# Kernel tuning notes

Measured on AMD Instinct MI355X. Metric: run time of the kernel, lower is better.

## Reference

```python
import jax, jax.numpy as jnp
import numpy as np

EMB = 256
HEADS = 2
IMG = 224
P1, P2 = 16, 8
LN_EPS = 1e-5


def _layer_norm(t, g, b):
    m = jnp.mean(t, axis=-1, keepdims=True)
    v = jnp.mean((t - m) ** 2, axis=-1, keepdims=True)
    return (t - m) * jax.lax.rsqrt(v + LN_EPS) * g + b


def _patch_embed(x, W, b, cls_tok, p):
    B, C, H, Wd = x.shape
    h, w = H // p, Wd // p
    # b c (h p1)(w p2) -> b (h w) (p1 p2 c)
    t = x.reshape(B, C, h, p, w, p).transpose(0, 2, 4, 3, 5, 1).reshape(B, h * w, p * p * C)
    t = t @ W + b
    cls = jnp.broadcast_to(cls_tok, (B, 1, cls_tok.shape[-1]))
    return jnp.concatenate([cls, t], axis=1)


def setup_inputs() -> dict:
    key = jax.random.key(0)
    ks = jax.random.split(key, 16)
    s = 0.02
    d = {
        "x": jax.random.normal(ks[0], (128, 3, IMG, IMG), dtype=jnp.float32),
        "W1": jax.random.normal(ks[1], (P1 * P1 * 3, EMB), dtype=jnp.float32) * s,
        "b1": jnp.zeros((EMB,), jnp.float32),
        "cls1": jax.random.normal(ks[2], (1, 1, EMB), dtype=jnp.float32),
        "W2": jax.random.normal(ks[3], (P2 * P2 * 3, EMB), dtype=jnp.float32) * s,
        "b2": jnp.zeros((EMB,), jnp.float32),
        "cls2": jax.random.normal(ks[4], (1, 1, EMB), dtype=jnp.float32),
        "ln1_g": jnp.ones((EMB,), jnp.float32),
        "ln1_b": jnp.zeros((EMB,), jnp.float32),
        "Wq": jax.random.normal(ks[5], (EMB, EMB), dtype=jnp.float32) * s,
        "bq": jnp.zeros((EMB,), jnp.float32),
        "Wk": jax.random.normal(ks[6], (EMB, EMB), dtype=jnp.float32) * s,
        "bk": jnp.zeros((EMB,), jnp.float32),
        "Wv": jax.random.normal(ks[7], (EMB, EMB), dtype=jnp.float32) * s,
        "bv": jnp.zeros((EMB,), jnp.float32),
        "Wp": jax.random.normal(ks[8], (EMB, EMB), dtype=jnp.float32) * s,
        "bp": jnp.zeros((EMB,), jnp.float32),
        "ln2_g": jnp.ones((EMB,), jnp.float32),
        "ln2_b": jnp.zeros((EMB,), jnp.float32),
        "lnc_g": jnp.ones((EMB,), jnp.float32),
        "lnc_b": jnp.zeros((EMB,), jnp.float32),
        "Wc": jax.random.normal(ks[9], (EMB, 2), dtype=jnp.float32) * s,
        "bc": jnp.zeros((2,), jnp.float32),
    }
    return d


def reference(x, W1, b1, cls1, W2, b2, cls2, ln1_g, ln1_b, Wq, bq, Wk, bk, Wv, bv,
              Wp, bp, ln2_g, ln2_b, lnc_g, lnc_b, Wc, bc):
    B = x.shape[0]
    p1 = _patch_embed(x, W1, b1, cls1, P1)   # [B, 197, 256]
    p2 = _patch_embed(x, W2, b2, cls2, P2)   # [B, 785, 256]
    n = p1.shape[1]
    idx = jnp.linspace(0.0, p2.shape[1] - 1, n).astype(jnp.int32)  # truncation like .long()
    p2r = p2[:, idx, :]
    z = jnp.concatenate([p2r, p1], axis=1)   # [B, 394, 256]
    N = z.shape[1]

    h = _layer_norm(z, ln1_g, ln1_b)
    dh = EMB // HEADS
    q = (h @ Wq + bq).reshape(B, N, HEADS, dh).transpose(0, 2, 1, 3)
    k = (h @ Wk + bk).reshape(B, N, HEADS, dh).transpose(0, 2, 1, 3)
    v = (h @ Wv + bv).reshape(B, N, HEADS, dh).transpose(0, 2, 1, 3)
    attn = jnp.einsum('bhqd,bhkd->bhqk', q, k)
    # NOTE: faithful to source — softmax of UNscaled logits, then divide by sqrt(emb)
    attn = jax.nn.softmax(attn, axis=-1) / (EMB ** 0.5)
    o = jnp.einsum('bhqk,bhkd->bhqd', attn, v).transpose(0, 2, 1, 3).reshape(B, N, EMB)
    o = o @ Wp + bp
    o = _layer_norm(o, ln2_g, ln2_b)
    z = z + o

    pooled = jnp.mean(z, axis=1)
    logits = _layer_norm(pooled, lnc_g, lnc_b) @ Wc + bc
    return jax.nn.log_softmax(logits, axis=1)
```

## Files before the change

kernel.cpp:

```cpp
#include <hip/hip_runtime.h>

typedef short short8 __attribute__((ext_vector_type(8)));
typedef float f32x4 __attribute__((ext_vector_type(4)));
typedef unsigned short us4 __attribute__((ext_vector_type(4)));
typedef unsigned short u16;

#define MFMA(a,b,c) __builtin_amdgcn_mfma_f32_16x16x32_bf16((a),(b),(c),0,0,0)

__device__ __forceinline__ u16 f2b(float f) {
    union { float f; unsigned int i; } v; v.f = f;
    unsigned int x = v.i;
    return (u16)((x + 0x7fffu + ((x >> 16) & 1u)) >> 16);
}

__device__ __forceinline__ unsigned int pk2(float lo, float hi) {
    return (unsigned int)f2b(lo) | ((unsigned int)f2b(hi) << 16);
}

__global__ __launch_bounds__(256) void k_wtrans(const float* __restrict__ W1,
        const float* __restrict__ W2, const float* __restrict__ Wq, const float* __restrict__ Wk,
        const float* __restrict__ Wv, const float* __restrict__ Wp,
        u16* __restrict__ w1t, u16* __restrict__ w2t, u16* __restrict__ wqt,
        u16* __restrict__ wkt, u16* __restrict__ wvt, u16* __restrict__ wpt) {
    int bx = blockIdx.x, n = threadIdx.x;
    if (bx < 768) {
        int k = bx, c = k % 3, t = k / 3, pj = t & 15, pi = t >> 4;
        int kp2 = c*256 + pi*16 + pj;
        w1t[(size_t)(kp2 >> 5)*8192 + n*32 + (kp2 & 31)] = f2b(W1[(size_t)k*256 + n]);
    } else if (bx < 960) {
        int k = bx - 768, c = k % 3, t = k / 3, pj = t & 7, pi = t >> 3;
        int kp2 = c*64 + pi*8 + pj;
        w2t[(size_t)(kp2 >> 5)*8192 + n*32 + (kp2 & 31)] = f2b(W2[(size_t)k*256 + n]);
    } else if (bx < 1216) { int k = bx - 960;  wqt[(size_t)(k>>5)*8192 + n*32 + (k&31)] = f2b(Wq[(size_t)k*256 + n]); }
    else if (bx < 1472)   { int k = bx - 1216; wkt[(size_t)(k>>5)*8192 + n*32 + (k&31)] = f2b(Wk[(size_t)k*256 + n]); }
    else if (bx < 1728)   { int k = bx - 1472; wvt[(size_t)(k>>5)*8192 + n*32 + (k&31)] = f2b(Wv[(size_t)k*256 + n]); }
    else                  { int k = bx - 1728; wpt[(size_t)(k>>5)*8192 + n*32 + (k&31)] = f2b(Wp[(size_t)k*256 + n]); }
}

__global__ __launch_bounds__(256) void k_cls(const float* __restrict__ cls1,
        const float* __restrict__ cls2, const float* __restrict__ g1, const float* __restrict__ be1,
        float* __restrict__ z, u16* __restrict__ h) {
    __shared__ float red[16];
    int b = blockIdx.x, e = threadIdx.x, lane = e & 63, w = e >> 6;
    float v0 = cls2[e], v1 = cls1[e];
    z[((size_t)b*394 + 0)*256 + e]   = v0;
    z[((size_t)b*394 + 197)*256 + e] = v1;
    float s0 = v0, q0 = v0*v0, s1 = v1, q1 = v1*v1;
    #pragma unroll
    for (int m = 1; m < 64; m <<= 1) {
        s0 += __shfl_xor(s0, m); q0 += __shfl_xor(q0, m);
        s1 += __shfl_xor(s1, m); q1 += __shfl_xor(q1, m);
    }
    if (lane == 0) { red[w] = s0; red[4+w] = q0; red[8+w] = s1; red[12+w] = q1; }
    __syncthreads();
    float S0 = red[0]+red[1]+red[2]+red[3],   Q0 = red[4]+red[5]+red[6]+red[7];
    float S1 = red[8]+red[9]+red[10]+red[11], Q1 = red[12]+red[13]+red[14]+red[15];
    float m0 = S0*(1.f/256.f), r0 = rsqrtf(Q0*(1.f/256.f) - m0*m0 + 1e-5f);
    float m1 = S1*(1.f/256.f), r1 = rsqrtf(Q1*(1.f/256.f) - m1*m1 + 1e-5f);
    h[((size_t)b*394 + 0)*256 + e]   = f2b((v0-m0)*r0*g1[e] + be1[e]);
    h[((size_t)b*394 + 197)*256 + e] = f2b((v1-m1)*r1*g1[e] + be1[e]);
}

__global__ __launch_bounds__(256) void k_im2col1(const float* __restrict__ x,
        u16* __restrict__ A1) {
    int b = blockIdx.y, g = blockIdx.x, tid = threadIdx.x;
    int p = tid >> 4, pi = tid & 15;
    int j = g*16 + p;
    u16* dst = A1 + ((size_t)b*208 + j)*768;
    if (j < 196) {
        int hi = j / 14, wi = j - hi*14;
        #pragma unroll
        for (int c = 0; c < 3; ++c) {
            const float* src = x + (((size_t)b*3 + c)*224 + hi*16 + pi)*224 + wi*16;
            f32x4 r0 = *(const f32x4*)(src);
            f32x4 r1 = *(const f32x4*)(src + 4);
            f32x4 r2 = *(const f32x4*)(src + 8);
            f32x4 r3 = *(const f32x4*)(src + 12);
            union { u16 u[16]; uint4 q[2]; } t;
            #pragma unroll
            for (int s = 0; s < 4; ++s) {
                t.u[s] = f2b(r0[s]); t.u[4+s] = f2b(r1[s]);
                t.u[8+s] = f2b(r2[s]); t.u[12+s] = f2b(r3[s]);
            }
            *(uint4*)&dst[c*256 + pi*16] = t.q[0];
            *(uint4*)&dst[c*256 + pi*16 + 8] = t.q[1];
        }
    } else {
        uint4 zer = {0,0,0,0};
        #pragma unroll
        for (int c = 0; c < 3; ++c) {
            *(uint4*)&dst[c*256 + pi*16] = zer;
            *(uint4*)&dst[c*256 + pi*16 + 8] = zer;
        }
    }
}

__global__ __launch_bounds__(256) void k_embed1(const u16* __restrict__ A1,
        const u16* __restrict__ w1t, const float* __restrict__ b1,
        const float* __restrict__ g1, const float* __restrict__ be1,
        float* __restrict__ z, u16* __restrict__ h, int nrows) {
    __shared__ __align__(16) u16 Ab[2][64*40];
    __shared__ __align__(16) u16 Bb[2][256*40];
    __shared__ float red[64][8];
    int tid = threadIdx.x;
    int r0 = blockIdx.x * 64;
    int w = tid >> 6, lane = tid & 63, quad = lane >> 4, tf = lane & 15;
    int arow = tid >> 2, aoff = (tid & 3) * 8;
    const u16* ap = A1 + (size_t)(r0 + arow)*768 + aoff;
    uint4 ra  = *(const uint4*)(ap);
    uint4 rb0 = *(const uint4*)&w1t[tid*8];
    uint4 rb1 = *(const uint4*)&w1t[2048 + tid*8];
    uint4 rb2 = *(const uint4*)&w1t[4096 + tid*8];
    uint4 rb3 = *(const uint4*)&w1t[6144 + tid*8];
    f32x4 zero = {0.f,0.f,0.f,0.f};
    f32x4 acc[4][4];
    #pragma unroll
    for (int m = 0; m < 4; ++m)
        #pragma unroll
        for (int nf = 0; nf < 4; ++nf) acc[m][nf] = zero;
    #pragma unroll
    for (int kc = 0; kc < 24; ++kc) {
        int buf = kc & 1;
        *(uint4*)&Ab[buf][arow*40 + aoff] = ra;
        *(uint4*)&Bb[buf][(arow      )*40 + aoff] = rb0;
        *(uint4*)&Bb[buf][(arow +  64)*40 + aoff] = rb1;
        *(uint4*)&Bb[buf][(arow + 128)*40 + aoff] = rb2;
        *(uint4*)&Bb[buf][(arow + 192)*40 + aoff] = rb3;
        int nc = kc < 23 ? kc + 1 : 23;
        ra = *(const uint4*)(ap + nc*32);
        const u16* src = w1t + (size_t)nc*8192;
        rb0 = *(const uint4*)&src[tid*8];
        rb1 = *(const uint4*)&src[2048 + tid*8];
        rb2 = *(const uint4*)&src[4096 + tid*8];
        rb3 = *(const uint4*)&src[6144 + tid*8];
        __syncthreads();
        short8 a0 = *(const short8*)&Ab[buf][(     tf)*40 + quad*8];
        short8 a1 = *(const short8*)&Ab[buf][(16 + tf)*40 + quad*8];
        short8 a2 = *(const short8*)&Ab[buf][(32 + tf)*40 + quad*8];
        short8 a3 = *(const short8*)&Ab[buf][(48 + tf)*40 + quad*8];
        #pragma unroll
        for (int nf = 0; nf < 4; ++nf) {
            short8 bb = *(const short8*)&Bb[buf][(w*64 + nf*16 + tf)*40 + quad*8];
            acc[0][nf] = MFMA(a0, bb, acc[0][nf]);
            acc[1][nf] = MFMA(a1, bb, acc[1][nf]);
            acc[2][nf] = MFMA(a2, bb, acc[2][nf]);
            acc[3][nf] = MFMA(a3, bb, acc[3][nf]);
        }
    }
    float bias[4], gv[4], bev[4];
    #pragma unroll
    for (int nf = 0; nf < 4; ++nf) {
        int n = w*64 + nf*16 + tf;
        bias[nf] = b1[n]; gv[nf] = g1[n]; bev[nf] = be1[n];
    }
    #pragma unroll
    for (int m = 0; m < 4; ++m)
        #pragma unroll
        for (int nf = 0; nf < 4; ++nf)
            #pragma unroll
            for (int i = 0; i < 4; ++i) acc[m][nf][i] += bias[nf];
    #pragma unroll
    for (int m = 0; m < 4; ++m)
        #pragma unroll
        for (int i = 0; i < 4; ++i) {
            float s = acc[m][0][i] + acc[m][1][i] + acc[m][2][i] + acc[m][3][i];
            float qv = acc[m][0][i]*acc[m][0][i] + acc[m][1][i]*acc[m][1][i]
                     + acc[m][2][i]*acc[m][2][i] + acc[m][3][i]*acc[m][3][i];
            #pragma unroll
            for (int d = 1; d < 16; d <<= 1) { s += __shfl_xor(s, d); qv += __shfl_xor(qv, d); }
            if (tf == 0) {
                red[m*16 + quad*4 + i][w] = s;
                red[m*16 + quad*4 + i][4 + w] = qv;
            }
        }
    __syncthreads();
    #pragma unroll
    for (int m = 0; m < 4; ++m)
        #pragma unroll
        for (int i = 0; i < 4; ++i) {
            int rl = m*16 + quad*4 + i;
            float S = red[rl][0]+red[rl][1]+red[rl][2]+red[rl][3];
            float Q = red[rl][4]+red[rl][5]+red[rl][6]+red[rl][7];
            float mean = S*(1.f/256.f);
            float rs = rsqrtf(Q*(1.f/256.f) - mean*mean + 1e-5f);
            int row = r0 + rl;
            if (row < nrows) {
                int img = row / 208;
                int j = row - img*208;
                if (j < 196) {
                    size_t base = ((size_t)img*394 + 198 + j)*256;
                    #pragma unroll
                    for (int nf = 0; nf < 4; ++nf) {
                        int n = w*64 + nf*16 + tf;
                        float v = acc[m][nf][i];
                        z[base + n] = v;
                        h[base + n] = f2b((v - mean)*rs*gv[nf] + bev[nf]);
                    }
                }
            }
        }
}

__global__ __launch_bounds__(256) void k_embed2(const float* __restrict__ x,
        const u16* __restrict__ w2t, const float* __restrict__ b2,
        const float* __restrict__ g1, const float* __restrict__ be1,
        float* __restrict__ z, u16* __restrict__ h) {
    __shared__ __align__(16) u16 A[16*200];
    __shared__ __align__(16) u16 Wst[8192];
    __shared__ __align__(16) float S[16*260];
    int b = blockIdx.y, g = blockIdx.x, tid = threadIdx.x;
    int p = tid >> 4, s16 = tid & 15;
    int pi = s16 >> 1, ph = s16 & 1;
    int it = g*16 + p + 1;
    uint4 wr0 = *(const uint4*)&w2t[tid*8];
    uint4 wr1 = *(const uint4*)&w2t[2048 + tid*8];
    uint4 wr2 = *(const uint4*)&w2t[4096 + tid*8];
    uint4 wr3 = *(const uint4*)&w2t[6144 + tid*8];
    auto stage = [&](const u16* base, int chunk) {
        __syncthreads();
        *(uint4*)&Wst[tid*8] = wr0;
        *(uint4*)&Wst[2048 + tid*8] = wr1;
        *(uint4*)&Wst[4096 + tid*8] = wr2;
        *(uint4*)&Wst[6144 + tid*8] = wr3;
        __syncthreads();
        if (base) {
            const u16* src = base + (size_t)chunk*8192;
            wr0 = *(const uint4*)&src[tid*8];
            wr1 = *(const uint4*)&src[2048 + tid*8];
            wr2 = *(const uint4*)&src[4096 + tid*8];
            wr3 = *(const uint4*)&src[6144 + tid*8];
        }
    };
    if (it <= 196) {
        int patch = 4*it - 1;
        int hi = patch / 28, wi = patch - hi*28;
        #pragma unroll
        for (int c = 0; c < 3; ++c) {
            const float* src = x + (((size_t)b*3 + c)*224 + hi*8 + pi)*224 + wi*8 + ph*4;
            f32x4 r = *(const f32x4*)src;
            us4 o; o[0] = f2b(r[0]); o[1] = f2b(r[1]); o[2] = f2b(r[2]); o[3] = f2b(r[3]);
            *(us4*)&A[p*200 + c*64 + pi*8 + ph*4] = o;
        }
    } else {
        us4 zer = {0,0,0,0};
        #pragma unroll
        for (int c = 0; c < 3; ++c)
            *(us4*)&A[p*200 + c*64 + pi*8 + ph*4] = zer;
    }
    int w = tid >> 6, lane = tid & 63, quad = lane >> 4, tf = lane & 15;
    f32x4 zero = {0.f,0.f,0.f,0.f};
    f32x4 acc[4] = {zero,zero,zero,zero};
    #pragma unroll
    for (int ks = 0; ks < 6; ++ks) {
        stage(ks < 5 ? w2t : nullptr, ks + 1);
        short8 a = *(const short8*)&A[tf*200 + ks*32 + quad*8];
        #pragma unroll
        for (int nf = 0; nf < 4; ++nf) {
            short8 bb = *(const short8*)&Wst[(w*64 + nf*16 + tf)*32 + quad*8];
            acc[nf] = MFMA(a, bb, acc[nf]);
        }
    }
    #pragma unroll
    for (int nf = 0; nf < 4; ++nf) {
        int n = w*64 + nf*16 + tf;
        float bias = b2[n];
        #pragma unroll
        for (int i = 0; i < 4; ++i)
            S[(quad*4 + i)*260 + n] = acc[nf][i] + bias;
    }
    __syncthreads();
    #pragma unroll
    for (int rr = 0; rr < 4; ++rr) {
        int row = w*4 + rr;
        int it2 = g*16 + row + 1;
        f32x4 v = *(const f32x4*)&S[row*260 + lane*4];
        float s = v[0]+v[1]+v[2]+v[3];
        float sq = v[0]*v[0]+v[1]*v[1]+v[2]*v[2]+v[3]*v[3];
        #pragma unroll
        for (int m = 1; m < 64; m <<= 1) { s += __shfl_xor(s, m); sq += __shfl_xor(sq, m); }
        float mean = s*(1.f/256.f);
        float rs = rsqrtf(sq*(1.f/256.f) - mean*mean + 1e-5f);
        if (it2 <= 196) {
            size_t base = ((size_t)b*394 + it2)*256 + lane*4;
            *(f32x4*)&z[base] = v;
            us4 ho;
            #pragma unroll
            for (int c = 0; c < 4; ++c) {
                int e = lane*4 + c;
                ho[c] = f2b((v[c]-mean)*rs*g1[e] + be1[e]);
            }
            *(us4*)&h[base] = ho;
        }
    }
}

__device__ __forceinline__ void store_qk(f32x4 acc[4][4], const float* __restrict__ bs,
        u16* __restrict__ dst, u16* Sst, int b, int mt, int w, int quad, int tf, int tid) {
    #pragma unroll
    for (int m = 0; m < 4; ++m) {
        __syncthreads();
        #pragma unroll
        for (int nf = 0; nf < 4; ++nf) {
            int e = w*64 + nf*16 + tf;
            float bias = bs[e];
            #pragma unroll
            for (int i = 0; i < 4; ++i) {
                int n = mt*64 + m*16 + quad*4 + i;
                Sst[(quad*4 + i)*264 + e] = (n < 394) ? f2b(acc[m][nf][i] + bias) : (u16)0;
            }
        }
        __syncthreads();
        int row = tid >> 4, c16 = tid & 15;
        int n = mt*64 + m*16 + row;
        if (n < 416) {
            int e0 = c16*16, hh = e0 >> 7, d0 = e0 & 127;
            uint4 v0 = *(const uint4*)&Sst[row*264 + e0];
            uint4 v1 = *(const uint4*)&Sst[row*264 + e0 + 8];
            u16* p = dst + ((size_t)(b*2 + hh)*416 + n)*128 + d0;
            *(uint4*)p = v0;
            *(uint4*)(p + 8) = v1;
        }
    }
}

__device__ __forceinline__ void store_v(f32x4 acc[4][4], const float* __restrict__ bs,
        u16* __restrict__ vt, u16* Sst, int b, int mt, int w, int quad, int tf, int tid) {
    #pragma unroll
    for (int nf = 0; nf < 4; ++nf) {
        __syncthreads();
        #pragma unroll
        for (int i = 0; i < 4; ++i) {
            int e = w*64 + nf*16 + quad*4 + i;
            float bias = bs[e];
            #pragma unroll
            for (int m = 0; m < 4; ++m) {
                int n = mt*64 + m*16 + tf;
                Sst[(w*16 + quad*4 + i)*72 + m*16 + tf] = (n < 394) ? f2b(acc[m][nf][i] + bias) : (u16)0;
            }
        }
        __syncthreads();
        #pragma unroll
        for (int k = 0; k < 2; ++k) {
            int ch = tid + k*256;
            int row = ch >> 3, c8 = ch & 7;
            int n0 = mt*64 + c8*8;
            if (n0 < 416) {
                int e = (row >> 4)*64 + nf*16 + (row & 15);
                int d = e & 127, hh = e >> 7;
                uint4 v = *(const uint4*)&Sst[row*72 + c8*8];
                *(uint4*)&vt[((size_t)(b*2 + hh)*128 + d)*416 + n0] = v;
            }
        }
    }
}

__global__ __launch_bounds__(256) void k_qkv(const u16* __restrict__ h,
        const u16* __restrict__ wqt, const u16* __restrict__ wkt, const u16* __restrict__ wvt,
        const float* __restrict__ bq, const float* __restrict__ bk, const float* __restrict__ bv,
        u16* __restrict__ q, u16* __restrict__ kb, u16* __restrict__ vt) {
    __shared__ __align__(16) u16 A[64*264];
    __shared__ __align__(16) u16 Wst[2][8192];
    __shared__ __align__(16) u16 Sst[4608];
    int mt = blockIdx.x, b = blockIdx.y, tid = threadIdx.x;
    auto cptr = [&](int i) -> const u16* {
        return i < 8 ? wqt + (size_t)i*8192
             : i < 16 ? wkt + (size_t)(i-8)*8192
                      : wvt + (size_t)(i-16)*8192;
    };
    uint4 wa0, wa1, wa2, wa3;
    uint4 wb0, wb1, wb2, wb3;
    auto loadA = [&](const u16* src) {
        wa0 = *(const uint4*)&src[tid*8];
        wa1 = *(const uint4*)&src[2048 + tid*8];
        wa2 = *(const uint4*)&src[4096 + tid*8];
        wa3 = *(const uint4*)&src[6144 + tid*8];
    };
    auto loadB = [&](const u16* src) {
        wb0 = *(const uint4*)&src[tid*8];
        wb1 = *(const uint4*)&src[2048 + tid*8];
        wb2 = *(const uint4*)&src[4096 + tid*8];
        wb3 = *(const uint4*)&src[6144 + tid*8];
    };
    auto writeA = [&]() {
        *(uint4*)&Wst[0][tid*8] = wa0;
        *(uint4*)&Wst[0][2048 + tid*8] = wa1;
        *(uint4*)&Wst[0][4096 + tid*8] = wa2;
        *(uint4*)&Wst[0][6144 + tid*8] = wa3;
    };
    auto writeB = [&]() {
        *(uint4*)&Wst[1][tid*8] = wb0;
        *(uint4*)&Wst[1][2048 + tid*8] = wb1;
        *(uint4*)&Wst[1][4096 + tid*8] = wb2;
        *(uint4*)&Wst[1][6144 + tid*8] = wb3;
    };
    loadA(cptr(0));
    loadB(cptr(1));
    #pragma unroll
    for (int it = 0; it < 8; ++it) {
        int idx = tid + it*256;
        int row = idx >> 5, seg = idx & 31;
        int n = mt*64 + row;
        uint4 val = {0,0,0,0};
        if (n < 394) val = *(const uint4*)&h[((size_t)b*394 + n)*256 + seg*8];
        *(uint4*)&A[row*264 + seg*8] = val;
    }
    int w = tid >> 6, lane = tid & 63, quad = lane >> 4, tf = lane & 15;
    f32x4 zero = {0.f,0.f,0.f,0.f};

    {
        f32x4 acc[4][4];
        #pragma unroll
        for (int m = 0; m < 4; ++m)
            #pragma unroll
            for (int nf = 0; nf < 4; ++nf) acc[m][nf] = zero;
        #pragma unroll
        for (int ks = 0; ks < 8; ++ks) {
            int i = ks, buf = ks & 1;
            if (buf == 0) writeA(); else writeB();
            if (i + 2 < 24) { if (buf == 0) loadA(cptr(i + 2)); else loadB(cptr(i + 2)); }
            __syncthreads();
            short8 a0 = *(const short8*)&A[tf*264 + ks*32 + quad*8];
            short8 a1 = *(const short8*)&A[(16+tf)*264 + ks*32 + quad*8];
            short8 a2 = *(const short8*)&A[(32+tf)*264 + ks*32 + quad*8];
            short8 a3 = *(const short8*)&A[(48+tf)*264 + ks*32 + quad*8];
            #pragma unroll
            for (int nf = 0; nf < 4; ++nf) {
                short8 bb = *(const short8*)&Wst[buf][(w*64 + nf*16 + tf)*32 + quad*8];
                acc[0][nf] = MFMA(a0, bb, acc[0][nf]);
                acc[1][nf] = MFMA(a1, bb, acc[1][nf]);
                acc[2][nf] = MFMA(a2, bb, acc[2][nf]);
                acc[3][nf] = MFMA(a3, bb, acc[3][nf]);
            }
        }
        store_qk(acc, bq, q, Sst, b, mt, w, quad, tf, tid);
    }
    {
        f32x4 acc[4][4];
        #pragma unroll
        for (int m = 0; m < 4; ++m)
            #pragma unroll
            for (int nf = 0; nf < 4; ++nf) acc[m][nf] = zero;
        #pragma unroll
        for (int ks = 0; ks < 8; ++ks) {
            int i = 8 + ks, buf = ks & 1;
            if (buf == 0) writeA(); else writeB();
            if (i + 2 < 24) { if (buf == 0) loadA(cptr(i + 2)); else loadB(cptr(i + 2)); }
            __syncthreads();
            short8 a0 = *(const short8*)&A[tf*264 + ks*32 + quad*8];
            short8 a1 = *(const short8*)&A[(16+tf)*264 + ks*32 + quad*8];
            short8 a2 = *(const short8*)&A[(32+tf)*264 + ks*32 + quad*8];
            short8 a3 = *(const short8*)&A[(48+tf)*264 + ks*32 + quad*8];
            #pragma unroll
            for (int nf = 0; nf < 4; ++nf) {
                short8 bb = *(const short8*)&Wst[buf][(w*64 + nf*16 + tf)*32 + quad*8];
                acc[0][nf] = MFMA(a0, bb, acc[0][nf]);
                acc[1][nf] = MFMA(a1, bb, acc[1][nf]);
                acc[2][nf] = MFMA(a2, bb, acc[2][nf]);
                acc[3][nf] = MFMA(a3, bb, acc[3][nf]);
            }
        }
        store_qk(acc, bk, kb, Sst, b, mt, w, quad, tf, tid);
    }
    {
        f32x4 acc[4][4];
        #pragma unroll
        for (int m = 0; m < 4; ++m)
            #pragma unroll
            for (int nf = 0; nf < 4; ++nf) acc[m][nf] = zero;
        #pragma unroll
        for (int ks = 0; ks < 8; ++ks) {
            int i = 16 + ks, buf = ks & 1;
            if (buf == 0) writeA(); else writeB();
            if (i + 2 < 24) { if (buf == 0) loadA(cptr(i + 2)); else loadB(cptr(i + 2)); }
            __syncthreads();
            short8 a0 = *(const short8*)&A[tf*264 + ks*32 + quad*8];
            short8 a1 = *(const short8*)&A[(16+tf)*264 + ks*32 + quad*8];
            short8 a2 = *(const short8*)&A[(32+tf)*264 + ks*32 + quad*8];
            short8 a3 = *(const short8*)&A[(48+tf)*264 + ks*32 + quad*8];
            #pragma unroll
            for (int nf = 0; nf < 4; ++nf) {
                short8 bb = *(const short8*)&Wst[buf][(w*64 + nf*16 + tf)*32 + quad*8];
                acc[0][nf] = MFMA(bb, a0, acc[0][nf]);
                acc[1][nf] = MFMA(bb, a1, acc[1][nf]);
                acc[2][nf] = MFMA(bb, a2, acc[2][nf]);
                acc[3][nf] = MFMA(bb, a3, acc[3][nf]);
            }
        }
        store_v(acc, bv, vt, Sst, b, mt, w, quad, tf, tid);
    }
}

__global__ __launch_bounds__(256) void k_att(const u16* __restrict__ q,
        const u16* __restrict__ kbuf, const u16* __restrict__ vt, u16* __restrict__ o) {
    __shared__ __align__(16) u16 pool[18944];
    int nwg = gridDim.x * gridDim.y;
    int orig = blockIdx.y * gridDim.x + blockIdx.x;
    int q8 = nwg >> 3, r8 = nwg & 7;
    int xcd = orig & 7, idx = orig >> 3;
    int nid = (xcd < r8 ? xcd*(q8+1) : r8*(q8+1) + (xcd-r8)*q8) + idx;
    int bx = nid % 7, bh = nid / 7;
    int tid = threadIdx.x;
    int w = tid >> 6, lane = tid & 63, quad = lane >> 4, tf = lane & 15;
    int mt_raw = bx*4 + w;
    int mt = mt_raw < 26 ? mt_raw : 25;
    const u16* qp = q    + (size_t)bh*53248;
    const u16* kp = kbuf + (size_t)bh*53248;
    const u16* vp = vt   + (size_t)bh*53248;
    short8 afr[4];
    #pragma unroll
    for (int ks = 0; ks < 4; ++ks)
        afr[ks] = *(const short8*)&qp[(size_t)(mt*16 + tf)*128 + ks*32 + quad*8];
    f32x4 zero = {0.f,0.f,0.f,0.f};
    f32x4 acc[25];
    #pragma unroll
    for (int nt = 0; nt < 25; ++nt) acc[nt] = zero;
    int sr0 = tid >> 4, sseg = tid & 15;
    uint4 kreg0 = *(const uint4*)&kp[(size_t)sr0*128 + sseg*8];
    uint4 kreg1 = *(const uint4*)&kp[(size_t)(sr0+16)*128 + sseg*8];
    for (int kc = 0; kc < 13; ++kc) {
        u16* K = pool + (kc & 1)*4352;
        *(uint4*)&K[sr0*136 + sseg*8] = kreg0;
        *(uint4*)&K[(sr0+16)*136 + sseg*8] = kreg1;
        if (kc < 12) {
            kreg0 = *(const uint4*)&kp[(size_t)((kc+1)*32 + sr0)*128 + sseg*8];
            kreg1 = *(const uint4*)&kp[(size_t)((kc+1)*32 + sr0 + 16)*128 + sseg*8];
        }
        __syncthreads();
        #pragma unroll
        for (int ncl = 0; ncl < 2; ++ncl) {
            int nt = kc*2 + ncl;
            if (nt < 25) {
                #pragma unroll
                for (int ks = 0; ks < 4; ++ks) {
                    short8 kk = *(const short8*)&K[(ncl*16 + tf)*136 + ks*32 + quad*8];
                    acc[nt] = MFMA(kk, afr[ks], acc[nt]);
                }
            }
        }
    }
    int vd0 = tid >> 2, vseg = tid & 3;
    uint4 vreg0 = *(const uint4*)&vp[(size_t)vd0*416 + vseg*8];
    uint4 vreg1 = *(const uint4*)&vp[(size_t)(vd0+64)*416 + vseg*8];
    float mx = -3e38f;
    #pragma unroll
    for (int nt = 0; nt < 24; ++nt)
        #pragma unroll
        for (int i = 0; i < 4; ++i) mx = fmaxf(mx, acc[nt][i]);
    #pragma unroll
    for (int i = 0; i < 4; ++i)
        if (quad*4 + i < 10) mx = fmaxf(mx, acc[24][i]);
    mx = fmaxf(mx, __shfl_xor(mx, 16));
    mx = fmaxf(mx, __shfl_xor(mx, 32));
    float s = 0.f;
    #pragma unroll
    for (int nt = 0; nt < 24; ++nt)
        #pragma unroll
        for (int i = 0; i < 4; ++i) {
            float e = __expf(acc[nt][i] - mx);
            acc[nt][i] = e; s += e;
        }
    #pragma unroll
    for (int i = 0; i < 4; ++i) {
        if (quad*4 + i < 10) { float e = __expf(acc[24][i] - mx); acc[24][i] = e; s += e; }
        else acc[24][i] = 0.f;
    }
    s += __shfl_xor(s, 16);
    s += __shfl_xor(s, 32);
    float inv = 1.f / (16.f * s);
    #pragma unroll
    for (int nt = 0; nt < 25; ++nt)
        #pragma unroll
        for (int i = 0; i < 4; ++i) acc[nt][i] *= inv;
    f32x4 acc2[8];
    #pragma unroll
    for (int nf = 0; nf < 8; ++nf) acc2[nf] = zero;
    int qb0 = quad & 1;
    int g = (qb0 << 1) | (quad >> 1);
    for (int kc = 0; kc < 13; ++kc) {
        u16* V = pool + 8704 + (kc & 1)*5120;
        *(uint4*)&V[vd0*40 + vseg*8] = vreg0;
        *(uint4*)&V[(vd0+64)*40 + vseg*8] = vreg1;
        if (kc < 12) {
            vreg0 = *(const uint4*)&vp[(size_t)vd0*416 + (kc+1)*32 + vseg*8];
            vreg1 = *(const uint4*)&vp[(size_t)(vd0+64)*416 + (kc+1)*32 + vseg*8];
        }
        __syncthreads();
        f32x4 v0 = acc[2*kc];
        f32x4 v1 = (kc < 12) ? acc[2*kc + 1] : zero;
        unsigned int r0 = pk2(v0[0], v0[1]);
        unsigned int r1 = pk2(v0[2], v0[3]);
        unsigned int r2 = pk2(v1[0], v1[1]);
        unsigned int r3 = pk2(v1[2], v1[3]);
        unsigned int sa = qb0 ? r0 : r2, sb = qb0 ? r1 : r3;
        unsigned int ra = (unsigned int)__shfl_xor((int)sa, 16);
        unsigned int rb = (unsigned int)__shfl_xor((int)sb, 16);
        unsigned int ka = qb0 ? r2 : r0, kb2 = qb0 ? r3 : r1;
        union { unsigned int u[4]; short8 s8; } au;
        au.u[0] = qb0 ? ra : ka;
        au.u[1] = qb0 ? rb : kb2;
        au.u[2] = qb0 ? ka : ra;
        au.u[3] = qb0 ? kb2 : rb;
        short8 a = au.s8;
        #pragma unroll
        for (int nf = 0; nf < 8; ++nf) {
            short8 bb = *(const short8*)&V[(nf*16 + tf)*40 + g*8];
            acc2[nf] = MFMA(a, bb, acc2[nf]);
        }
    }
    int b = bh >> 1, hh = bh & 1;
    __syncthreads();
    #pragma unroll
    for (int nf = 0; nf < 8; ++nf)
        #pragma unroll
        for (int i = 0; i < 4; ++i)
            pool[w*2176 + (quad*4 + i)*136 + nf*16 + tf] = f2b(acc2[nf][i]);
    __syncthreads();
    if (mt_raw < 26) {
        #pragma unroll
        for (int r4 = 0; r4 < 4; ++r4) {
            int rr = r4*4 + (lane >> 4);
            int n = mt_raw*16 + rr;
            if (n < 394) {
                int c16 = lane & 15;
                uint4 v = *(const uint4*)&pool[w*2176 + rr*136 + c16*8];
                *(uint4*)&o[((size_t)b*394 + n)*256 + hh*128 + c16*8] = v;
            }
        }
    }
}

__global__ __launch_bounds__(256) void k_proj(const u16* __restrict__ o,
        const u16* __restrict__ wpt, const float* __restrict__ bp,
        const float* __restrict__ g2, const float* __restrict__ bb2,
        float* __restrict__ z) {
    __shared__ __align__(16) u16 A[32*264];
    __shared__ __align__(16) u16 Wst[8192];
    __shared__ __align__(16) float S[32*260];
    int mt = blockIdx.x, b = blockIdx.y, tid = threadIdx.x;
    int w = tid >> 6, lane = tid & 63, quad = lane >> 4, tf = lane & 15;
    uint4 wr0 = *(const uint4*)&wpt[tid*8];
    uint4 wr1 = *(const uint4*)&wpt[2048 + tid*8];
    uint4 wr2 = *(const uint4*)&wpt[4096 + tid*8];
    uint4 wr3 = *(const uint4*)&wpt[6144 + tid*8];
    auto stage = [&](const u16* base, int chunk) {
        __syncthreads();
        *(uint4*)&Wst[tid*8] = wr0;
        *(uint4*)&Wst[2048 + tid*8] = wr1;
        *(uint4*)&Wst[4096 + tid*8] = wr2;
        *(uint4*)&Wst[6144 + tid*8] = wr3;
        __syncthreads();
        if (base) {
            const u16* src = base + (size_t)chunk*8192;
            wr0 = *(const uint4*)&src[tid*8];
            wr1 = *(const uint4*)&src[2048 + tid*8];
            wr2 = *(const uint4*)&src[4096 + tid*8];
            wr3 = *(const uint4*)&src[6144 + tid*8];
        }
    };
    for (int idx = tid; idx < 2048; idx += 256) {
        int row = idx >> 6, col4 = (idx & 63) * 4;
        int n = mt*32 + row;
        us4 val = {0,0,0,0};
        if (n < 394) val = *(const us4*)&o[((size_t)b*394 + n)*256 + col4];
        *(us4*)&A[row*264 + col4] = val;
    }
    f32x4 zero = {0.f,0.f,0.f,0.f};
    f32x4 acc[2][4];
    #pragma unroll
    for (int m = 0; m < 2; ++m)
        #pragma unroll
        for (int nf = 0; nf < 4; ++nf) acc[m][nf] = zero;
    #pragma unroll
    for (int ks = 0; ks < 8; ++ks) {
        stage(ks < 7 ? wpt : nullptr, ks + 1);
        short8 a0 = *(const short8*)&A[tf*264 + ks*32 + quad*8];
        short8 a1 = *(const short8*)&A[(16+tf)*264 + ks*32 + quad*8];
        #pragma unroll
        for (int nf = 0; nf < 4; ++nf) {
            short8 bb = *(const short8*)&Wst[(w*64 + nf*16 + tf)*32 + quad*8];
            acc[0][nf] = MFMA(a0, bb, acc[0][nf]);
            acc[1][nf] = MFMA(a1, bb, acc[1][nf]);
        }
    }
    #pragma unroll
    for (int nf = 0; nf < 4; ++nf) {
        int e = w*64 + nf*16 + tf;
        float bsv = bp[e];
        #pragma unroll
        for (int m = 0; m < 2; ++m)
            #pragma unroll
            for (int i = 0; i < 4; ++i)
                S[(m*16 + quad*4 + i)*260 + e] = acc[m][nf][i] + bsv;
    }
    __syncthreads();
    #pragma unroll
    for (int rr = 0; rr < 8; ++rr) {
        int row = w*8 + rr;
        f32x4 v = *(const f32x4*)&S[row*260 + lane*4];
        float s = v[0]+v[1]+v[2]+v[3];
        float sq = v[0]*v[0]+v[1]*v[1]+v[2]*v[2]+v[3]*v[3];
        #pragma unroll
        for (int m = 1; m < 64; m <<= 1) { s += __shfl_xor(s, m); sq += __shfl_xor(sq, m); }
        float mean = s*(1.f/256.f);
        float rs = rsqrtf(sq*(1.f/256.f) - mean*mean + 1e-5f);
        int n = mt*32 + row;
        if (n < 394) {
            float* zr = z + ((size_t)b*394 + n)*256 + lane*4;
            f32x4 zv = *(f32x4*)zr;
            #pragma unroll
            for (int c = 0; c < 4; ++c) {
                int e = lane*4 + c;
                zv[c] += (v[c]-mean)*rs*g2[e] + bb2[e];
            }
            *(f32x4*)zr = zv;
        }
    }
}

__global__ __launch_bounds__(256) void k_poolsum(const float* __restrict__ z,
        float* __restrict__ partial) {
    int g = blockIdx.x, b = blockIdx.y, e = threadIdx.x;
    int nb = gridDim.y;
    int n0 = g*99, n1 = 394 < n0+99 ? 394 : n0+99;
    const float* zp = z + (size_t)b*394*256 + e;
    float p0 = 0.f, p1 = 0.f, p2 = 0.f, p3 = 0.f;
    int n = n0;
    for (; n + 3 < n1; n += 4) {
        p0 += zp[(size_t)n*256];       p1 += zp[(size_t)(n+1)*256];
        p2 += zp[(size_t)(n+2)*256];   p3 += zp[(size_t)(n+3)*256];
    }
    for (; n < n1; ++n) p0 += zp[(size_t)n*256];
    partial[((size_t)g*nb + b)*256 + e] = (p0+p1)+(p2+p3);
}

__global__ __launch_bounds__(256) void k_pool2(const float* __restrict__ partial,
        const float* __restrict__ lg, const float* __restrict__ lb,
        const float* __restrict__ wc, const float* __restrict__ bc,
        float* __restrict__ out, int nb) {
    __shared__ float red[8];
    int b = blockIdx.x, e = threadIdx.x;
    int wave = e >> 6, lane = e & 63;
    float pooled = (partial[((size_t)0*nb + b)*256 + e] + partial[((size_t)1*nb + b)*256 + e]
                  + partial[((size_t)2*nb + b)*256 + e] + partial[((size_t)3*nb + b)*256 + e])
                 * (1.f/394.f);
    float a = pooled, sq = pooled*pooled;
    #pragma unroll
    for (int m = 1; m < 64; m <<= 1) { a += __shfl_xor(a, m); sq += __shfl_xor(sq, m); }
    if (lane == 0) { red[wave] = a; red[4+wave] = sq; }
    __syncthreads();
    float tot = red[0]+red[1]+red[2]+red[3];
    float totq = red[4]+red[5]+red[6]+red[7];
    float mean = tot*(1.f/256.f);
    float rs = rsqrtf(totq*(1.f/256.f) - mean*mean + 1e-5f);
    float ln = (pooled-mean)*rs*lg[e] + lb[e];
    float t0 = ln * wc[e*2], t1 = ln * wc[e*2+1];
    #pragma unroll
    for (int m = 1; m < 64; m <<= 1) { t0 += __shfl_xor(t0, m); t1 += __shfl_xor(t1, m); }
    __syncthreads();
    if (lane == 0) { red[wave] = t0; red[4+wave] = t1; }
    __syncthreads();
    if (e < 2) {
        float l0 = red[0]+red[1]+red[2]+red[3] + bc[0];
        float l1 = red[4]+red[5]+red[6]+red[7] + bc[1];
        float mx = fmaxf(l0, l1);
        float lse = mx + logf(__expf(l0-mx) + __expf(l1-mx));
        out[b*2 + e] = (e == 0 ? l0 : l1) - lse;
    }
}

extern "C" void kernel_launch(void* const* d_in, const int* in_sizes, int n_in,
                              void* d_out, int out_size, void* d_ws, size_t ws_size,
                              hipStream_t stream) {
    const float* x    = (const float*)d_in[0];
    const float* W1   = (const float*)d_in[1];
    const float* b1   = (const float*)d_in[2];
    const float* cls1 = (const float*)d_in[3];
    const float* W2   = (const float*)d_in[4];
    const float* b2   = (const float*)d_in[5];
    const float* cls2 = (const float*)d_in[6];
    const float* ln1g = (const float*)d_in[7];
    const float* ln1b = (const float*)d_in[8];
    const float* Wq   = (const float*)d_in[9];
    const float* bq   = (const float*)d_in[10];
    const float* Wk   = (const float*)d_in[11];
    const float* bk   = (const float*)d_in[12];
    const float* Wv   = (const float*)d_in[13];
    const float* bv   = (const float*)d_in[14];
    const float* Wp   = (const float*)d_in[15];
    const float* bp   = (const float*)d_in[16];
    const float* ln2g = (const float*)d_in[17];
    const float* ln2b = (const float*)d_in[18];
    const float* lncg = (const float*)d_in[19];
    const float* lncb = (const float*)d_in[20];
    const float* Wc   = (const float*)d_in[21];
    const float* bcp  = (const float*)d_in[22];

    int Bn = in_sizes[0] / (3*224*224);

    const size_t WBYTES = 1015808;
    const size_t PER_IMG = 403456 + 201728 + 212992*3 + 4096;
    size_t avail = (ws_size > WBYTES) ? ws_size - WBYTES : 0;
    int Bc = (int)(avail / PER_IMG);
    if (Bc < 1) Bc = 1;
    if (Bc > Bn) Bc = Bn;

    u16* w1t = (u16*)d_ws;
    u16* w2t = w1t + 196608;
    u16* wqt = w2t + 49152;
    u16* wkt = wqt + 65536;
    u16* wvt = wkt + 65536;
    u16* wpt = wvt + 65536;
    float* z = (float*)(wpt + 65536);
    u16* h   = (u16*)(z + (size_t)Bc*100864);
    u16* o   = h;
    u16* q   = h + (size_t)Bc*100864;
    u16* kb  = q + (size_t)Bc*106496;
    u16* vt  = kb + (size_t)Bc*106496;
    float* partial = (float*)(vt + (size_t)Bc*106496);

    k_wtrans<<<1984, 256, 0, stream>>>(W1, W2, Wq, Wk, Wv, Wp, w1t, w2t, wqt, wkt, wvt, wpt);

    for (int b0 = 0; b0 < Bn; b0 += Bc) {
        int bc = (Bn - b0 < Bc) ? (Bn - b0) : Bc;
        const float* xb = x + (size_t)b0 * 3*224*224;
        float* outb = (float*)d_out + (size_t)b0 * 2;
        int nrows = bc * 208;
        int gm = (nrows + 63) / 64;

        k_cls<<<bc, 256, 0, stream>>>(cls1, cls2, ln1g, ln1b, z, h);
        k_im2col1<<<dim3(13, bc), 256, 0, stream>>>(xb, q );
        k_embed1<<<gm, 256, 0, stream>>>(q , w1t, b1, ln1g, ln1b, z, h, nrows);
        k_embed2<<<dim3(13, bc), 256, 0, stream>>>(xb, w2t, b2, ln1g, ln1b, z, h);
        k_qkv<<<dim3(7, bc), 256, 0, stream>>>(h, wqt, wkt, wvt, bq, bk, bv, q, kb, vt);
        k_att<<<dim3(7, bc*2), 256, 0, stream>>>(q, kb, vt, o);
        k_proj<<<dim3(13, bc), 256, 0, stream>>>(o, wpt, bp, ln2g, ln2b, z);
        k_poolsum<<<dim3(4, bc), 256, 0, stream>>>(z, partial);
        k_pool2<<<bc, 256, 0, stream>>>(partial, lncg, lncb, Wc, bcp, outb, bc);
    }
}
```

Baseline: 376.5 us.

## Fuse both im2col gathers and run embed2 as row-tiled GEMM like embed1

The im2col kernel now also gathers the 8x8 patches needed for the second embedding into a separate bf16 buffer, reusing the vt scratch. k_embed2 becomes a double-buffered 32-row-tile GEMM mirroring k_embed1 with an in-register LayerNorm reduction, replacing the per-image 16-row tile that staged the full weights with two syncs per k-step. k_embed1's row tile is halved from 64 to 32 rows to launch more blocks. This trades an extra global write and read of the A2 buffer, and more weight reloads per row, for better occupancy and fewer barriers.

```diff
diff --git a/kernel.cpp b/kernel.cpp
--- a/kernel.cpp
+++ b/kernel.cpp
@@ -61,14 +61,16 @@
     h[((size_t)b*394 + 197)*256 + e] = f2b((v1-m1)*r1*g1[e] + be1[e]);
 }
 
-__global__ __launch_bounds__(256) void k_im2col1(const float* __restrict__ x,
-        u16* __restrict__ A1) {
+__global__ __launch_bounds__(256) void k_im2col(const float* __restrict__ x,
+        u16* __restrict__ A1, u16* __restrict__ A2) {
     int b = blockIdx.y, g = blockIdx.x, tid = threadIdx.x;
-    int p = tid >> 4, pi = tid & 15;
+    int p = tid >> 4, s16 = tid & 15;
     int j = g*16 + p;
-    u16* dst = A1 + ((size_t)b*208 + j)*768;
+    u16* dst  = A1 + ((size_t)b*208 + j)*768;
+    u16* dst2 = A2 + ((size_t)b*208 + j)*192;
     if (j < 196) {
         int hi = j / 14, wi = j - hi*14;
+        int pi = s16;
         #pragma unroll
         for (int c = 0; c < 3; ++c) {
             const float* src = x + (((size_t)b*3 + c)*224 + hi*16 + pi)*224 + wi*16;
@@ -85,12 +87,25 @@
             *(uint4*)&dst[c*256 + pi*16] = t.q[0];
             *(uint4*)&dst[c*256 + pi*16 + 8] = t.q[1];
         }
+        int patch = 4*j + 3;
+        int hi2 = patch / 28, wi2 = patch - hi2*28;
+        int pi2 = s16 >> 1, ph = s16 & 1;
+        #pragma unroll
+        for (int c = 0; c < 3; ++c) {
+            const float* src = x + (((size_t)b*3 + c)*224 + hi2*8 + pi2)*224 + wi2*8 + ph*4;
+            f32x4 r = *(const f32x4*)src;
+            us4 o; o[0] = f2b(r[0]); o[1] = f2b(r[1]); o[2] = f2b(r[2]); o[3] = f2b(r[3]);
+            *(us4*)&dst2[c*64 + pi2*8 + ph*4] = o;
+        }
     } else {
-        uint4 zer = {0,0,0,0};
+        uint4 zer4 = {0,0,0,0};
+        us4 zer = {0,0,0,0};
+        int pi = s16, pi2 = s16 >> 1, ph = s16 & 1;
         #pragma unroll
         for (int c = 0; c < 3; ++c) {
-            *(uint4*)&dst[c*256 + pi*16] = zer;
-            *(uint4*)&dst[c*256 + pi*16 + 8] = zer;
+            *(uint4*)&dst[c*256 + pi*16] = zer4;
+            *(uint4*)&dst[c*256 + pi*16 + 8] = zer4;
+            *(us4*)&dst2[c*64 + pi2*8 + ph*4] = zer;
         }
     }
 }
@@ -99,35 +114,36 @@
         const u16* __restrict__ w1t, const float* __restrict__ b1,
         const float* __restrict__ g1, const float* __restrict__ be1,
         float* __restrict__ z, u16* __restrict__ h, int nrows) {
-    __shared__ __align__(16) u16 Ab[2][64*40];
+    __shared__ __align__(16) u16 Ab[2][32*40];
     __shared__ __align__(16) u16 Bb[2][256*40];
-    __shared__ float red[64][8];
+    __shared__ float red[32][8];
     int tid = threadIdx.x;
-    int r0 = blockIdx.x * 64;
+    int r0 = blockIdx.x * 32;
     int w = tid >> 6, lane = tid & 63, quad = lane >> 4, tf = lane & 15;
-    int arow = tid >> 2, aoff = (tid & 3) * 8;
-    const u16* ap = A1 + (size_t)(r0 + arow)*768 + aoff;
-    uint4 ra  = *(const uint4*)(ap);
+    int arow = tid >> 3, aseg = (tid & 7) * 4;
+    int brow = tid >> 2, boff = (tid & 3) * 8;
+    const u16* ap = A1 + (size_t)(r0 + arow)*768 + aseg;
+    uint2 ra  = *(const uint2*)(ap);
     uint4 rb0 = *(const uint4*)&w1t[tid*8];
     uint4 rb1 = *(const uint4*)&w1t[2048 + tid*8];
     uint4 rb2 = *(const uint4*)&w1t[4096 + tid*8];
     uint4 rb3 = *(const uint4*)&w1t[6144 + tid*8];
     f32x4 zero = {0.f,0.f,0.f,0.f};
-    f32x4 acc[4][4];
-    #pragma unroll
-    for (int m = 0; m < 4; ++m)
+    f32x4 acc[2][4];
+    #pragma unroll
+    for (int m = 0; m < 2; ++m)
         #pragma unroll
         for (int nf = 0; nf < 4; ++nf) acc[m][nf] = zero;
     #pragma unroll
     for (int kc = 0; kc < 24; ++kc) {
         int buf = kc & 1;
-        *(uint4*)&Ab[buf][arow*40 + aoff] = ra;
-        *(uint4*)&Bb[buf][(arow      )*40 + aoff] = rb0;
-        *(uint4*)&Bb[buf][(arow +  64)*40 + aoff] = rb1;
-        *(uint4*)&Bb[buf][(arow + 128)*40 + aoff] = rb2;
-        *(uint4*)&Bb[buf][(arow + 192)*40 + aoff] = rb3;
+        *(uint2*)&Ab[buf][arow*40 + aseg] = ra;
+        *(uint4*)&Bb[buf][(brow      )*40 + boff] = rb0;
+        *(uint4*)&Bb[buf][(brow +  64)*40 + boff] = rb1;
+        *(uint4*)&Bb[buf][(brow + 128)*40 + boff] = rb2;
+        *(uint4*)&Bb[buf][(brow + 192)*40 + boff] = rb3;
         int nc = kc < 23 ? kc + 1 : 23;
-        ra = *(const uint4*)(ap + nc*32);
+        ra = *(const uint2*)(ap + nc*32);
         const u16* src = w1t + (size_t)nc*8192;
         rb0 = *(const uint4*)&src[tid*8];
         rb1 = *(const uint4*)&src[2048 + tid*8];
@@ -136,15 +152,11 @@
         __syncthreads();
         short8 a0 = *(const short8*)&Ab[buf][(     tf)*40 + quad*8];
         short8 a1 = *(const short8*)&Ab[buf][(16 + tf)*40 + quad*8];
-        short8 a2 = *(const short8*)&Ab[buf][(32 + tf)*40 + quad*8];
-        short8 a3 = *(const short8*)&Ab[buf][(48 + tf)*40 + quad*8];
         #pragma unroll
         for (int nf = 0; nf < 4; ++nf) {
             short8 bb = *(const short8*)&Bb[buf][(w*64 + nf*16 + tf)*40 + quad*8];
             acc[0][nf] = MFMA(a0, bb, acc[0][nf]);
             acc[1][nf] = MFMA(a1, bb, acc[1][nf]);
-            acc[2][nf] = MFMA(a2, bb, acc[2][nf]);
-            acc[3][nf] = MFMA(a3, bb, acc[3][nf]);
         }
     }
     float bias[4], gv[4], bev[4];
@@ -154,13 +166,13 @@
         bias[nf] = b1[n]; gv[nf] = g1[n]; bev[nf] = be1[n];
     }
     #pragma unroll
-    for (int m = 0; m < 4; ++m)
+    for (int m = 0; m < 2; ++m)
         #pragma unroll
         for (int nf = 0; nf < 4; ++nf)
             #pragma unroll
             for (int i = 0; i < 4; ++i) acc[m][nf][i] += bias[nf];
     #pragma unroll
-    for (int m = 0; m < 4; ++m)
+    for (int m = 0; m < 2; ++m)
         #pragma unroll
         for (int i = 0; i < 4; ++i) {
             float s = acc[m][0][i] + acc[m][1][i] + acc[m][2][i] + acc[m][3][i];
@@ -175,7 +187,7 @@
         }
     __syncthreads();
     #pragma unroll
-    for (int m = 0; m < 4; ++m)
+    for (int m = 0; m < 2; ++m)
         #pragma unroll
         for (int i = 0; i < 4; ++i) {
             int rl = m*16 + quad*4 + i;
@@ -201,97 +213,107 @@
         }
 }
 
-__global__ __launch_bounds__(256) void k_embed2(const float* __restrict__ x,
+__global__ __launch_bounds__(256) void k_embed2(const u16* __restrict__ A2,
         const u16* __restrict__ w2t, const float* __restrict__ b2,
         const float* __restrict__ g1, const float* __restrict__ be1,
-        float* __restrict__ z, u16* __restrict__ h) {
-    __shared__ __align__(16) u16 A[16*200];
-    __shared__ __align__(16) u16 Wst[8192];
-    __shared__ __align__(16) float S[16*260];
-    int b = blockIdx.y, g = blockIdx.x, tid = threadIdx.x;
-    int p = tid >> 4, s16 = tid & 15;
-    int pi = s16 >> 1, ph = s16 & 1;
-    int it = g*16 + p + 1;
-    uint4 wr0 = *(const uint4*)&w2t[tid*8];
-    uint4 wr1 = *(const uint4*)&w2t[2048 + tid*8];
-    uint4 wr2 = *(const uint4*)&w2t[4096 + tid*8];
-    uint4 wr3 = *(const uint4*)&w2t[6144 + tid*8];
-    auto stage = [&](const u16* base, int chunk) {
-        __syncthreads();
-        *(uint4*)&Wst[tid*8] = wr0;
-        *(uint4*)&Wst[2048 + tid*8] = wr1;
-        *(uint4*)&Wst[4096 + tid*8] = wr2;
-        *(uint4*)&Wst[6144 + tid*8] = wr3;
-        __syncthreads();
-        if (base) {
-            const u16* src = base + (size_t)chunk*8192;
-            wr0 = *(const uint4*)&src[tid*8];
-            wr1 = *(const uint4*)&src[2048 + tid*8];
-            wr2 = *(const uint4*)&src[4096 + tid*8];
-            wr3 = *(const uint4*)&src[6144 + tid*8];
-        }
-    };
-    if (it <= 196) {
-        int patch = 4*it - 1;
-        int hi = patch / 28, wi = patch - hi*28;
-        #pragma unroll
-        for (int c = 0; c < 3; ++c) {
-            const float* src = x + (((size_t)b*3 + c)*224 + hi*8 + pi)*224 + wi*8 + ph*4;
-            f32x4 r = *(const f32x4*)src;
-            us4 o; o[0] = f2b(r[0]); o[1] = f2b(r[1]); o[2] = f2b(r[2]); o[3] = f2b(r[3]);
-            *(us4*)&A[p*200 + c*64 + pi*8 + ph*4] = o;
-        }
-    } else {
-        us4 zer = {0,0,0,0};
-        #pragma unroll
-        for (int c = 0; c < 3; ++c)
-            *(us4*)&A[p*200 + c*64 + pi*8 + ph*4] = zer;
-    }
+        float* __restrict__ z, u16* __restrict__ h, int nrows) {
+    __shared__ __align__(16) u16 Ab[2][32*40];
+    __shared__ __align__(16) u16 Bb[2][256*40];
+    __shared__ float red[32][8];
+    int tid = threadIdx.x;
+    int r0 = blockIdx.x * 32;
     int w = tid >> 6, lane = tid & 63, quad = lane >> 4, tf = lane & 15;
+    int arow = tid >> 3, aseg = (tid & 7) * 4;
+    int brow = tid >> 2, boff = (tid & 3) * 8;
+    const u16* ap = A2 + (size_t)(r0 + arow)*192 + aseg;
+    uint2 ra  = *(const uint2*)(ap);
+    uint4 rb0 = *(const uint4*)&w2t[tid*8];
+    uint4 rb1 = *(const uint4*)&w2t[2048 + tid*8];
+    uint4 rb2 = *(const uint4*)&w2t[4096 + tid*8];
+    uint4 rb3 = *(const uint4*)&w2t[6144 + tid*8];
     f32x4 zero = {0.f,0.f,0.f,0.f};
-    f32x4 acc[4] = {zero,zero,zero,zero};
-    #pragma unroll
-    for (int ks = 0; ks < 6; ++ks) {
-        stage(ks < 5 ? w2t : nullptr, ks + 1);
-        short8 a = *(const short8*)&A[tf*200 + ks*32 + quad*8];
+    f32x4 acc[2][4];
+    #pragma unroll
+    for (int m = 0; m < 2; ++m)
+        #pragma unroll
+        for (int nf = 0; nf < 4; ++nf) acc[m][nf] = zero;
+    #pragma unroll
+    for (int kc = 0; kc < 6; ++kc) {
+        int buf = kc & 1;
+        *(uint2*)&Ab[buf][arow*40 + aseg] = ra;
+        *(uint4*)&Bb[buf][(brow      )*40 + boff] = rb0;
+        *(uint4*)&Bb[buf][(brow +  64)*40 + boff] = rb1;
+        *(uint4*)&Bb[buf][(brow + 128)*40 + boff] = rb2;
+        *(uint4*)&Bb[buf][(brow + 192)*40 + boff] = rb3;
+        int nc = kc < 5 ? kc + 1 : 5;
+        ra = *(const uint2*)(ap + nc*32);
+        const u16* src = w2t + (size_t)nc*8192;
+        rb0 = *(const uint4*)&src[tid*8];
+        rb1 = *(const uint4*)&src[2048 + tid*8];
+        rb2 = *(const uint4*)&src[4096 + tid*8];
+        rb3 = *(const uint4*)&src[6144 + tid*8];
+        __syncthreads();
+        short8 a0 = *(const short8*)&Ab[buf][(     tf)*40 + quad*8];
+        short8 a1 = *(const short8*)&Ab[buf][(16 + tf)*40 + quad*8];
         #pragma unroll
         for (int nf = 0; nf < 4; ++nf) {
-            short8 bb = *(const short8*)&Wst[(w*64 + nf*16 + tf)*32 + quad*8];
-            acc[nf] = MFMA(a, bb, acc[nf]);
-        }
-    }
+            short8 bb = *(const short8*)&Bb[buf][(w*64 + nf*16 + tf)*40 + quad*8];
+            acc[0][nf] = MFMA(a0, bb, acc[0][nf]);
+            acc[1][nf] = MFMA(a1, bb, acc[1][nf]);
+        }
+    }
+    float bias[4], gv[4], bev[4];
     #pragma unroll
     for (int nf = 0; nf < 4; ++nf) {
         int n = w*64 + nf*16 + tf;
-        float bias = b2[n];
-        #pragma unroll
-        for (int i = 0; i < 4; ++i)
-            S[(quad*4 + i)*260 + n] = acc[nf][i] + bias;
-    }
+        bias[nf] = b2[n]; gv[nf] = g1[n]; bev[nf] = be1[n];
+    }
+    #pragma unroll
+    for (int m = 0; m < 2; ++m)
+        #pragma unroll
+        for (int nf = 0; nf < 4; ++nf)
+            #pragma unroll
+            for (int i = 0; i < 4; ++i) acc[m][nf][i] += bias[nf];
+    #pragma unroll
+    for (int m = 0; m < 2; ++m)
+        #pragma unroll
+        for (int i = 0; i < 4; ++i) {
+            float s = acc[m][0][i] + acc[m][1][i] + acc[m][2][i] + acc[m][3][i];
+            float qv = acc[m][0][i]*acc[m][0][i] + acc[m][1][i]*acc[m][1][i]
+                     + acc[m][2][i]*acc[m][2][i] + acc[m][3][i]*acc[m][3][i];
+            #pragma unroll
+            for (int d = 1; d < 16; d <<= 1) { s += __shfl_xor(s, d); qv += __shfl_xor(qv, d); }
+            if (tf == 0) {
+                red[m*16 + quad*4 + i][w] = s;
+                red[m*16 + quad*4 + i][4 + w] = qv;
+            }
+        }
     __syncthreads();
     #pragma unroll
-    for (int rr = 0; rr < 4; ++rr) {
-        int row = w*4 + rr;
-        int it2 = g*16 + row + 1;
-        f32x4 v = *(const f32x4*)&S[row*260 + lane*4];
-        float s = v[0]+v[1]+v[2]+v[3];
-        float sq = v[0]*v[0]+v[1]*v[1]+v[2]*v[2]+v[3]*v[3];
-        #pragma unroll
-        for (int m = 1; m < 64; m <<= 1) { s += __shfl_xor(s, m); sq += __shfl_xor(sq, m); }
-        float mean = s*(1.f/256.f);
-        float rs = rsqrtf(sq*(1.f/256.f) - mean*mean + 1e-5f);
-        if (it2 <= 196) {
-            size_t base = ((size_t)b*394 + it2)*256 + lane*4;
-            *(f32x4*)&z[base] = v;
-            us4 ho;
-            #pragma unroll
-            for (int c = 0; c < 4; ++c) {
-                int e = lane*4 + c;
-                ho[c] = f2b((v[c]-mean)*rs*g1[e] + be1[e]);
-            }
-            *(us4*)&h[base] = ho;
-        }
-    }
+    for (int m = 0; m < 2; ++m)
+        #pragma unroll
+        for (int i = 0; i < 4; ++i) {
+            int rl = m*16 + quad*4 + i;
+            float S = red[rl][0]+red[rl][1]+red[rl][2]+red[rl][3];
+            float Q = red[rl][4]+red[rl][5]+red[rl][6]+red[rl][7];
+            float mean = S*(1.f/256.f);
+            float rs = rsqrtf(Q*(1.f/256.f) - mean*mean + 1e-5f);
+            int row = r0 + rl;
+            if (row < nrows) {
+                int img = row / 208;
+                int j = row - img*208;
+                if (j < 196) {
+                    size_t base = ((size_t)img*394 + 1 + j)*256;
+                    #pragma unroll
+                    for (int nf = 0; nf < 4; ++nf) {
+                        int n = w*64 + nf*16 + tf;
+                        float v = acc[m][nf][i];
+                        z[base + n] = v;
+                        h[base + n] = f2b((v - mean)*rs*gv[nf] + bev[nf]);
+                    }
+                }
+            }
+        }
 }
 
 __device__ __forceinline__ void store_qk(f32x4 acc[4][4], const float* __restrict__ bs,
@@ -825,12 +847,12 @@
         const float* xb = x + (size_t)b0 * 3*224*224;
         float* outb = (float*)d_out + (size_t)b0 * 2;
         int nrows = bc * 208;
-        int gm = (nrows + 63) / 64;
+        int gm = (nrows + 31) / 32;
 
         k_cls<<<bc, 256, 0, stream>>>(cls1, cls2, ln1g, ln1b, z, h);
-        k_im2col1<<<dim3(13, bc), 256, 0, stream>>>(xb, q );
+        k_im2col<<<dim3(13, bc), 256, 0, stream>>>(xb, q , vt );
         k_embed1<<<gm, 256, 0, stream>>>(q , w1t, b1, ln1g, ln1b, z, h, nrows);
-        k_embed2<<<dim3(13, bc), 256, 0, stream>>>(xb, w2t, b2, ln1g, ln1b, z, h);
+        k_embed2<<<gm, 256, 0, stream>>>(vt , w2t, b2, ln1g, ln1b, z, h, nrows);
         k_qkv<<<dim3(7, bc), 256, 0, stream>>>(h, wqt, wkt, wvt, bq, bk, bv, q, kb, vt);
         k_att<<<dim3(7, bc*2), 256, 0, stream>>>(q, kb, vt, o);
         k_proj<<<dim3(13, bc), 256, 0, stream>>>(o, wpt, bp, ln2g, ln2b, z);
```

Result: slower. 387.2 us (+2.9%).
